# Optimization experiments

Hardware: AMD Instinct MI355X
Metric: run time of the kernel (lower is better)

## Reference

```python
import jax, jax.numpy as jnp
import numpy as np

E = 16      # num_experts
K = 2       # top-k
C = 1280    # capacity = ceil(8192*2/16*1.25)


def setup_inputs() -> dict:
    key = jax.random.key(0)
    ks = jax.random.split(key, 7)
    B, T, D, F, DFF = 4, 2048, 1024, 512, 512
    s = 0.02
    return {
        "hidden_state": jax.random.normal(ks[0], (B, T, D), jnp.float32),
        "router_w": jax.random.normal(ks[1], (D, E), jnp.float32) * s,
        "shared_gate_w": jax.random.normal(ks[2], (D, 1), jnp.float32) * s,
        "w1": jax.random.normal(ks[3], (E, D, F), jnp.float32) * s,
        "w2": jax.random.normal(ks[4], (E, F, D), jnp.float32) * s,
        "sw1": jax.random.normal(ks[5], (D, DFF), jnp.float32) * s,
        "sw2": jax.random.normal(ks[6], (DFF, D), jnp.float32) * s,
    }


def reference(hidden_state, router_w, shared_gate_w, w1, w2, sw1, sw2):
    B, T, D = hidden_state.shape
    N = B * T
    # Router: softmax over expert logits + shared sigmoid gate
    logits = jnp.einsum("btd,de->bte", hidden_state, router_w)
    scores = jax.nn.softmax(logits, axis=-1)                      # [B,T,E]
    g_shared = jax.nn.sigmoid(jnp.einsum("btd,do->bto", hidden_state, shared_gate_w))

    topk_vals, topk_idx = jax.lax.top_k(scores, K)                # [B,T,K]
    x = hidden_state.reshape(N, D)
    token_for_route = jnp.repeat(jnp.arange(N), K)                # [N*K]
    expert_for_route = topk_idx.reshape(-1)                       # [N*K]
    gate_for_route = topk_vals.reshape(-1)                        # [N*K]

    # Stable sort by expert (jnp.argsort is stable)
    order = jnp.argsort(expert_for_route)
    expert_sorted = expert_for_route[order]
    token_sorted = token_for_route[order]
    gate_sorted = gate_for_route[order]
    x_sorted = x[token_sorted]                                    # [N*K, D]

    counts = jnp.bincount(expert_sorted, length=E)
    starts = jnp.cumsum(counts) - counts
    r = jnp.arange(N * K)
    positions = r - starts[expert_sorted]                         # slot within expert
    keep = (positions < C) & (gate_sorted != 0)
    p_idx = jnp.clip(positions, 0, C - 1)

    # Scatter kept tokens into fixed-capacity buffers; dropped routes go to dummy row E
    e_safe = jnp.where(keep, expert_sorted, E)
    p_safe = jnp.where(keep, p_idx, 0)
    buf = jnp.zeros((E + 1, C, D), x.dtype).at[e_safe, p_safe].set(
        jnp.where(keep[:, None], x_sorted, 0.0)
    )
    expert_inputs = buf[:E]                                       # [E,C,D]

    # Batched expert FFN (exact GELU, matching torch default)
    h = jax.nn.gelu(jnp.einsum("ech,ehf->ecf", expert_inputs, w1), approximate=False)
    expert_outputs = jnp.einsum("ecf,efh->ech", h, w2)            # [E,C,D]

    gate_eff = jnp.where(keep, gate_sorted, 0.0)
    y_sorted = expert_outputs[expert_sorted, p_idx] * gate_eff[:, None]

    # Combine: scatter-add back to tokens
    y_out = jnp.zeros((N, D), x.dtype).at[token_sorted].add(y_sorted).reshape(B, T, D)

    # Shared expert path
    shared_out = (jax.nn.gelu(x @ sw1, approximate=False) @ sw2).reshape(B, T, D)
    y_out = y_out + g_shared * shared_out

    # Stats (no attention_mask path)
    load_counts = jnp.bincount(expert_for_route, length=E)
    load = load_counts / (load_counts.sum() + 1e-12)
    importance = scores.mean(axis=(0, 1))
    return (y_out, importance, load)
```

## Files before the change

### kernel.cpp

```cpp
#include <hip/hip_runtime.h>
#include <hip/hip_bf16.h>
#include <math.h>

#define N_TOK 8192
#define DIM 1024
#define NEXP 16
#define CAP 1280
#define FDIM 512
#define NROUTE (N_TOK * 2)
#define NCHUNK 64
#define ECAP (NEXP * CAP)
#define TOTROW (ECAP + N_TOK)

typedef __hip_bfloat16 bf16;
typedef unsigned short ushort_t;
typedef __attribute__((ext_vector_type(8))) short bf16x8;
typedef __attribute__((ext_vector_type(4))) float f32x4;

__device__ __forceinline__ float gelu_fast(float x) {
    float u = 1.5957691216057308f * (x + 0.044715f * x * x * x);
    return x / (1.f + __expf(-u));
}

__device__ __forceinline__ float bf2f(unsigned short u) {
    union { float f; unsigned int i; } v; v.i = ((unsigned int)u) << 16; return v.f;
}

__device__ __forceinline__ unsigned short f2b(float f) {
    union { __hip_bfloat16 h; unsigned short u; } v;
    v.h = __float2bfloat16(f);
    return v.u;
}

__device__ __forceinline__ void gload16(const void* g, void* l) {
    __builtin_amdgcn_global_load_lds(
        (const __attribute__((address_space(1))) unsigned int*)g,
        (__attribute__((address_space(3))) unsigned int*)l,
        16, 0, 0);
}

__device__ __forceinline__ int swz_addr16(int r, int q) {
    return ((r >> 1) << 3) + ((r & 1) << 2) + (q ^ ((r >> 1) & 3));
}

#define PREP_RTR_BLOCKS 2048
#define PREP_NWG (PREP_RTR_BLOCKS + 2176)
__global__ __launch_bounds__(256) void prep_kernel(
    const float* __restrict__ x, const float* __restrict__ rw,
    const float* __restrict__ sgw,
    const float* __restrict__ w1, const float* __restrict__ w2,
    const float* __restrict__ sw1, const float* __restrict__ sw2,
    float* __restrict__ scores,
    int* __restrict__ topk_idx,
    float* __restrict__ topk_val,
    float* __restrict__ g_shared,
    ushort_t* __restrict__ x_bf,
    ushort_t* __restrict__ w1t, ushort_t* __restrict__ w2t,
    ushort_t* __restrict__ sw1t, ushort_t* __restrict__ sw2t)
{
    __shared__ union {
        ushort_t tileB[64][129];
        struct {
            float xl[4][1028];
            float racc[4][4][4][4];
            float g[4][4];
        } r;
    } sm;

    if (blockIdx.x < PREP_RTR_BLOCKS) {
        int tid = threadIdx.x;
        int w = tid >> 6;
        int lane = tid & 63;
        int tok0 = blockIdx.x * 4;

        {
            int dq = w * 256 + lane * 4;
            float4 gv = *reinterpret_cast<const float4*>(sgw + dq);
#pragma unroll
            for (int tt = 0; tt < 4; ++tt) {
                const float* xr = x + (size_t)(tok0 + tt) * DIM + dq;
                float4 xv = *reinterpret_cast<const float4*>(xr);
                *reinterpret_cast<float4*>(&sm.r.xl[tt][dq]) = xv;
                ushort4 o;
                o.x = f2b(xv.x); o.y = f2b(xv.y); o.z = f2b(xv.z); o.w = f2b(xv.w);
                *reinterpret_cast<ushort4*>(x_bf + (size_t)(tok0 + tt) * DIM + dq) = o;
                float dg = xv.x * gv.x + xv.y * gv.y + xv.z * gv.z + xv.w * gv.w;
#pragma unroll
                for (int m = 1; m < 64; m <<= 1) dg += __shfl_xor(dg, m, 64);
                if (lane == 0) sm.r.g[w][tt] = dg;
            }
        }
        __syncthreads();

        int tok = lane >> 4;
        int dup = (lane >> 2) & 3;
        int e4 = lane & 3;
        {
            int base_d = w * 256 + dup * 64;
            const float* rwb = rw + (size_t)base_d * NEXP + e4 * 4;
            float4 a0 = {0,0,0,0}, a1 = {0,0,0,0}, a2 = {0,0,0,0}, a3 = {0,0,0,0};
#pragma unroll 4
            for (int i = 0; i < 16; ++i) {
                float4 xv = *reinterpret_cast<const float4*>(&sm.r.xl[tok][base_d + i * 4]);
                const float* rp = rwb + (size_t)i * 4 * NEXP;
                float4 w0 = *reinterpret_cast<const float4*>(rp);
                float4 w1v = *reinterpret_cast<const float4*>(rp + NEXP);
                float4 w2v = *reinterpret_cast<const float4*>(rp + 2 * NEXP);
                float4 w3v = *reinterpret_cast<const float4*>(rp + 3 * NEXP);
                a0.x += xv.x * w0.x;  a0.y += xv.x * w0.y;  a0.z += xv.x * w0.z;  a0.w += xv.x * w0.w;
                a1.x += xv.y * w1v.x; a1.y += xv.y * w1v.y; a1.z += xv.y * w1v.z; a1.w += xv.y * w1v.w;
                a2.x += xv.z * w2v.x; a2.y += xv.z * w2v.y; a2.z += xv.z * w2v.z; a2.w += xv.z * w2v.w;
                a3.x += xv.w * w3v.x; a3.y += xv.w * w3v.y; a3.z += xv.w * w3v.z; a3.w += xv.w * w3v.w;
            }
            float s0 = (a0.x + a1.x) + (a2.x + a3.x);
            float s1 = (a0.y + a1.y) + (a2.y + a3.y);
            float s2 = (a0.z + a1.z) + (a2.z + a3.z);
            float s3 = (a0.w + a1.w) + (a2.w + a3.w);
            s0 += __shfl_xor(s0, 4, 64);  s0 += __shfl_xor(s0, 8, 64);
            s1 += __shfl_xor(s1, 4, 64);  s1 += __shfl_xor(s1, 8, 64);
            s2 += __shfl_xor(s2, 4, 64);  s2 += __shfl_xor(s2, 8, 64);
            s3 += __shfl_xor(s3, 4, 64);  s3 += __shfl_xor(s3, 8, 64);
            if (dup == 0) {
                sm.r.racc[w][tok][e4][0] = s0;
                sm.r.racc[w][tok][e4][1] = s1;
                sm.r.racc[w][tok][e4][2] = s2;
                sm.r.racc[w][tok][e4][3] = s3;
            }
        }
        __syncthreads();

        if (tid >= 16) return;
        int tk = tid >> 2;
        int eq = tid & 3;
        int token = tok0 + tk;
        float L0 = sm.r.racc[0][tk][eq][0] + sm.r.racc[1][tk][eq][0]
                 + sm.r.racc[2][tk][eq][0] + sm.r.racc[3][tk][eq][0];
        float L1 = sm.r.racc[0][tk][eq][1] + sm.r.racc[1][tk][eq][1]
                 + sm.r.racc[2][tk][eq][1] + sm.r.racc[3][tk][eq][1];
        float L2 = sm.r.racc[0][tk][eq][2] + sm.r.racc[1][tk][eq][2]
                 + sm.r.racc[2][tk][eq][2] + sm.r.racc[3][tk][eq][2];
        float L3 = sm.r.racc[0][tk][eq][3] + sm.r.racc[1][tk][eq][3]
                 + sm.r.racc[2][tk][eq][3] + sm.r.racc[3][tk][eq][3];

        float mx = fmaxf(fmaxf(L0, L1), fmaxf(L2, L3));
        mx = fmaxf(mx, __shfl_xor(mx, 1, 4));
        mx = fmaxf(mx, __shfl_xor(mx, 2, 4));
        float P0 = expf(L0 - mx), P1 = expf(L1 - mx);
        float P2 = expf(L2 - mx), P3 = expf(L3 - mx);
        float s = (P0 + P1) + (P2 + P3);
        s += __shfl_xor(s, 1, 4);
        s += __shfl_xor(s, 2, 4);
        float inv = 1.f / s;
        P0 *= inv; P1 *= inv; P2 *= inv; P3 *= inv;

        float4 Pv = {P0, P1, P2, P3};
        *reinterpret_cast<float4*>(scores + (size_t)token * NEXP + eq * 4) = Pv;

        int base = eq * 4;
        float v = P0; int idx = base;
        if (P1 > v) { v = P1; idx = base + 1; }
        if (P2 > v) { v = P2; idx = base + 2; }
        if (P3 > v) { v = P3; idx = base + 3; }
#pragma unroll
        for (int m = 1; m < 4; m <<= 1) {
            float vo = __shfl_xor(v, m, 4);
            int io = __shfl_xor(idx, m, 4);
            if (vo > v || (vo == v && io < idx)) { v = vo; idx = io; }
        }
        int i0 = idx; float v0 = v;
        float q0 = (base + 0 == i0) ? -1.f : P0;
        float q1 = (base + 1 == i0) ? -1.f : P1;
        float q2 = (base + 2 == i0) ? -1.f : P2;
        float q3 = (base + 3 == i0) ? -1.f : P3;
        v = q0; idx = base;
        if (q1 > v) { v = q1; idx = base + 1; }
        if (q2 > v) { v = q2; idx = base + 2; }
        if (q3 > v) { v = q3; idx = base + 3; }
#pragma unroll
        for (int m = 1; m < 4; m <<= 1) {
            float vo = __shfl_xor(v, m, 4);
            int io = __shfl_xor(idx, m, 4);
            if (vo > v || (vo == v && io < idx)) { v = vo; idx = io; }
        }
        if (eq == 0) {
            topk_idx[2 * token] = i0; topk_idx[2 * token + 1] = idx;
            topk_val[2 * token] = v0; topk_val[2 * token + 1] = v;
            float ag = (sm.r.g[0][tk] + sm.r.g[1][tk]) + (sm.r.g[2][tk] + sm.r.g[3][tk]);
            g_shared[token] = 1.f / (1.f + expf(-ag));
        }
        return;
    }

    int bx = blockIdx.x - PREP_RTR_BLOCKS;
    const float* src; ushort_t* dst; int K, N, kt, nt;
    if (bx < 1024) {
        int e = bx >> 6, r = bx & 63;
        K = 1024; N = 512; kt = r >> 3; nt = r & 7;
        src = w1 + (size_t)e * K * N; dst = w1t + (size_t)e * K * N;
    } else if (bx < 2048) {
        int b2 = bx - 1024, e = b2 >> 6, r = b2 & 63;
        K = 512; N = 1024; kt = r >> 4; nt = r & 15;
        src = w2 + (size_t)e * K * N; dst = w2t + (size_t)e * K * N;
    } else if (bx < 2112) {
        int r = bx - 2048;
        K = 1024; N = 512; kt = r >> 3; nt = r & 7;
        src = sw1; dst = sw1t;
    } else {
        int r = bx - 2112;
        K = 512; N = 1024; kt = r >> 4; nt = r & 15;
        src = sw2; dst = sw2t;
    }
    int t = threadIdx.x;
#pragma unroll 4
    for (int i = 0; i < 8; ++i) {
        int u = t + 256 * i;
        int r = u >> 4;
        int c4 = (u & 15) * 4;
        float4 v = *reinterpret_cast<const float4*>(
            src + (size_t)(kt * 128 + r) * N + nt * 64 + c4);
        sm.tileB[c4 + 0][r] = f2b(v.x);
        sm.tileB[c4 + 1][r] = f2b(v.y);
        sm.tileB[c4 + 2][r] = f2b(v.z);
        sm.tileB[c4 + 3][r] = f2b(v.w);
    }
    __syncthreads();
#pragma unroll 4
    for (int i2 = 0; i2 < 4; ++i2) {
        int u = t + 256 * i2;
        int n = u >> 4;
        int kc = (u & 15) * 8;
        bf16x8 o;
#pragma unroll
        for (int j = 0; j < 8; ++j) o[j] = (short)sm.tileB[n][kc + j];
        *reinterpret_cast<bf16x8*>(dst + (size_t)(nt * 64 + n) * K + kt * 128 + kc) = o;
    }
}

__global__ __launch_bounds__(256) void hist_kernel(
    const int* __restrict__ topk_idx, int* __restrict__ chunk_hist)
{
    __shared__ int h[NEXP];
    int tid = threadIdx.x;
    if (tid < NEXP) h[tid] = 0;
    __syncthreads();
    int r = blockIdx.x * 256 + tid;
    atomicAdd(&h[topk_idx[r]], 1);
    __syncthreads();
    if (tid < NEXP) chunk_hist[blockIdx.x * NEXP + tid] = h[tid];
}

__global__ __launch_bounds__(64) void scan_kernel(
    const int* __restrict__ chunk_hist, int* __restrict__ chunk_off,
    int* __restrict__ counts_cap, float* __restrict__ out_tail)
{
    int e = threadIdx.x;
    if (e >= NEXP) return;
    int run = 0;
    for (int b = 0; b < NCHUNK; ++b) {
        chunk_off[b * NEXP + e] = run;
        run += chunk_hist[b * NEXP + e];
    }
    counts_cap[e] = run < CAP ? run : CAP;
    out_tail[NEXP + e] = (float)((double)run / 16384.0);
}

__global__ __launch_bounds__(256) void assign_kernel(
    const int* __restrict__ topk_idx, const float* __restrict__ topk_val,
    const int* __restrict__ chunk_off,
    int* __restrict__ route_slot, int* __restrict__ slot_token)
{
    __shared__ int wave_cnt[4][NEXP];
    int tid = threadIdx.x;
    int lane = tid & 63;
    int w = tid >> 6;
    int r = blockIdx.x * 256 + tid;
    int e = topk_idx[r];
    float gate = topk_val[r];
    int rank_w = 0;
#pragma unroll
    for (int e16 = 0; e16 < NEXP; ++e16) {
        unsigned long long bal = __ballot(e == e16);
        if (e == e16) rank_w = __popcll(bal & ((1ull << lane) - 1ull));
        if (lane == 0) wave_cnt[w][e16] = __popcll(bal);
    }
    __syncthreads();
    int rank = rank_w;
#pragma unroll
    for (int w2 = 0; w2 < 3; ++w2)
        if (w2 < w) rank += wave_cnt[w2][e];
    int pos = chunk_off[blockIdx.x * NEXP + e] + rank;
    int slot = -1;
    if (pos < CAP && gate != 0.f) {
        slot = e * CAP + pos;
        slot_token[slot] = r >> 1;
    }
    route_slot[r] = slot;
}

__global__ __launch_bounds__(256) void importance_kernel(
    const float* __restrict__ scores, float* __restrict__ out_tail)
{
    __shared__ float red[256];
    int e = blockIdx.x;
    float s = 0.f;
    for (int t = threadIdx.x; t < N_TOK; t += 256) s += scores[t * NEXP + e];
    red[threadIdx.x] = s;
    __syncthreads();
    for (int st = 128; st > 0; st >>= 1) {
        if (threadIdx.x < st) red[threadIdx.x] += red[threadIdx.x + st];
        __syncthreads();
    }
    if (threadIdx.x == 0) out_tail[e] = red[0] / (float)N_TOK;
}

#define G1_GX (NEXP * 5 + N_TOK / 256)
#define G1_NWG (G1_GX * (FDIM / 128))
__global__ __launch_bounds__(512) void gemm1_mfma(
    const ushort_t* __restrict__ x_bf,
    const ushort_t* __restrict__ w1t,
    const ushort_t* __restrict__ sw1t,
    const int* __restrict__ slot_token,
    const int* __restrict__ counts_cap,
    ushort_t* __restrict__ h_buf)
{
    __shared__ ushort_t As[3][256 * 32];
    __shared__ ushort_t Bs[3][128 * 32];

    int flat = blockIdx.x;
    int wg = (flat & 7) * (G1_NWG / 8) + (flat >> 3);
    int by = wg & 3;
    int bxg = wg >> 2;

    int g, rb;
    if (bxg < NEXP * 5) { g = bxg / 5; rb = bxg % 5; }
    else { g = NEXP; rb = bxg - NEXP * 5; }
    int Mg = (g < NEXP) ? counts_cap[g] : N_TOK;
    int m0 = rb * 256;
    if (m0 >= Mg) return;
    const ushort_t* Bt = (g < NEXP) ? (w1t + (size_t)g * DIM * FDIM) : sw1t;
    int n0 = by * 128;
    int t = threadIdx.x;

    const ushort_t* asrc[2];
    const ushort_t* bsrc;
#pragma unroll
    for (int i = 0; i < 2; ++i) {
        int s = t + i * 512;
        int lr = ((s >> 3) << 1) | ((s >> 2) & 1);
        int qq = (s & 3) ^ ((s >> 3) & 3);
        int row = m0 + lr;
        const ushort_t* base;
        if (g < NEXP) {
            int tok = (row < Mg) ? slot_token[g * CAP + row] : 0;
            if ((unsigned)tok >= N_TOK) tok = 0;
            base = x_bf + (size_t)tok * DIM;
        } else {
            base = x_bf + (size_t)row * DIM;
        }
        asrc[i] = base + qq * 8;
    }
    {
        int s = t;
        int lr = ((s >> 3) << 1) | ((s >> 2) & 1);
        int qq = (s & 3) ^ ((s >> 3) & 3);
        bsrc = Bt + (size_t)(n0 + lr) * DIM + qq * 8;
    }

    int lane = t & 63;
    int w = t >> 6;
    int wm = (w & 3) * 64, wn = (w >> 2) * 64;
    int l15 = lane & 15, q = lane >> 4;

    int aoff[4], boff[4];
#pragma unroll
    for (int m = 0; m < 4; ++m) aoff[m] = swz_addr16(wm + m * 16 + l15, q) << 3;
#pragma unroll
    for (int n = 0; n < 4; ++n) boff[n] = swz_addr16(wn + n * 16 + l15, q) << 3;

    f32x4 acc[4][4];
#pragma unroll
    for (int m = 0; m < 4; ++m)
#pragma unroll
        for (int n = 0; n < 4; ++n) acc[m][n] = (f32x4){0.f, 0.f, 0.f, 0.f};

    auto STAGE = [&](int buf, int koff) {
        gload16(asrc[0] + koff, &As[buf][t * 8]);
        gload16(asrc[1] + koff, &As[buf][t * 8 + 4096]);
        gload16(bsrc + koff, &Bs[buf][t * 8]);
    };

    const int NSTEP = DIM / 32;
    STAGE(0, 0);
    STAGE(1, 32);
    asm volatile("s_waitcnt vmcnt(3)" ::: "memory");
    __builtin_amdgcn_s_barrier();
    asm volatile("" ::: "memory");

    int cur = 0, b2 = 2;
    for (int kt = 0; kt < NSTEP; ++kt) {
        if (kt + 2 < NSTEP) STAGE(b2, (kt + 2) * 32);
        const ushort_t* asb = &As[cur][0];
        const ushort_t* bsb = &Bs[cur][0];
        bf16x8 af[4], bfr[4];
#pragma unroll
        for (int m = 0; m < 4; ++m)
            af[m] = *reinterpret_cast<const bf16x8*>(asb + aoff[m]);
#pragma unroll
        for (int n = 0; n < 4; ++n)
            bfr[n] = *reinterpret_cast<const bf16x8*>(bsb + boff[n]);
        __builtin_amdgcn_s_setprio(1);
#pragma unroll
        for (int m = 0; m < 4; ++m)
#pragma unroll
            for (int n = 0; n < 4; ++n)
                acc[m][n] = __builtin_amdgcn_mfma_f32_16x16x32_bf16(
                    af[m], bfr[n], acc[m][n], 0, 0, 0);
        __builtin_amdgcn_s_setprio(0);
        if (kt + 1 < NSTEP) {
            if (kt + 2 < NSTEP) asm volatile("s_waitcnt vmcnt(3)" ::: "memory");
            else                asm volatile("s_waitcnt vmcnt(0)" ::: "memory");
            __builtin_amdgcn_s_barrier();
            asm volatile("" ::: "memory");
        }
        cur = (cur == 2) ? 0 : cur + 1;
        b2  = (b2 == 2) ? 0 : b2 + 1;
    }

    size_t obase = ((g < NEXP) ? (size_t)g * CAP : (size_t)ECAP) + m0;
#pragma unroll
    for (int m = 0; m < 4; ++m) {
#pragma unroll
        for (int r = 0; r < 4; ++r) {
            int grow = wm + m * 16 + q * 4 + r;
            ushort_t* orow = h_buf + (obase + grow) * FDIM + n0 + wn + l15;
#pragma unroll
            for (int n = 0; n < 4; ++n)
                orow[n * 16] = f2b(gelu_fast(acc[m][n][r]));
        }
    }
}

#define G2_NWG (G1_GX * (DIM / 128))
__global__ __launch_bounds__(512) void gemm2_mfma(
    const ushort_t* __restrict__ h_buf,
    const ushort_t* __restrict__ w2t,
    const ushort_t* __restrict__ sw2t,
    const int* __restrict__ counts_cap,
    const float* __restrict__ g_shared,
    ushort_t* __restrict__ out_buf,
    ushort_t* __restrict__ sh_out)
{
    __shared__ ushort_t As[2][256 * 32];
    __shared__ ushort_t Bs[2][128 * 32];

    int flat = blockIdx.x;
    int wg = (flat & 7) * (G2_NWG / 8) + (flat >> 3);
    int by = wg & 7;
    int bxg = wg >> 3;

    int g, rb;
    if (bxg < NEXP * 5) { g = bxg / 5; rb = bxg % 5; }
    else { g = NEXP; rb = bxg - NEXP * 5; }
    int Mg = (g < NEXP) ? counts_cap[g] : N_TOK;
    int m0 = rb * 256;
    if (m0 >= Mg) return;
    size_t abase = ((g < NEXP) ? (size_t)g * CAP : (size_t)ECAP) + m0;
    const ushort_t* Bt = (g < NEXP) ? (w2t + (size_t)g * FDIM * DIM) : sw2t;
    int n0 = by * 128;
    int t = threadIdx.x;

    const ushort_t* asrc[2];
    const ushort_t* bsrc;
#pragma unroll
    for (int i = 0; i < 2; ++i) {
        int s = t + i * 512;
        int lr = ((s >> 3) << 1) | ((s >> 2) & 1);
        int qq = (s & 3) ^ ((s >> 3) & 3);
        asrc[i] = h_buf + (abase + lr) * FDIM + qq * 8;
    }
    {
        int s = t;
        int lr = ((s >> 3) << 1) | ((s >> 2) & 1);
        int qq = (s & 3) ^ ((s >> 3) & 3);
        bsrc = Bt + (size_t)(n0 + lr) * FDIM + qq * 8;
    }

    int lane = t & 63;
    int w = t >> 6;
    int wm = (w & 3) * 64, wn = (w >> 2) * 64;
    int l15 = lane & 15, q = lane >> 4;

    int aoff[4], boff[4];
#pragma unroll
    for (int m = 0; m < 4; ++m) aoff[m] = swz_addr16(wm + m * 16 + l15, q) << 3;
#pragma unroll
    for (int n = 0; n < 4; ++n) boff[n] = swz_addr16(wn + n * 16 + l15, q) << 3;

    f32x4 acc[4][4];
#pragma unroll
    for (int m = 0; m < 4; ++m)
#pragma unroll
        for (int n = 0; n < 4; ++n) acc[m][n] = (f32x4){0.f, 0.f, 0.f, 0.f};

    auto STAGE = [&](int buf, int koff) {
        gload16(asrc[0] + koff, &As[buf][t * 8]);
        gload16(asrc[1] + koff, &As[buf][t * 8 + 4096]);
        gload16(bsrc + koff, &Bs[buf][t * 8]);
    };

    const int NSTEP = FDIM / 32;
    STAGE(0, 0);
    __syncthreads();

    int cur = 0;
    for (int kt = 0; kt < NSTEP; ++kt) {
        if (kt + 1 < NSTEP) STAGE(cur ^ 1, (kt + 1) * 32);
        const ushort_t* asb = &As[cur][0];
        const ushort_t* bsb = &Bs[cur][0];
        bf16x8 af[4], bfr[4];
#pragma unroll
        for (int m = 0; m < 4; ++m)
            af[m] = *reinterpret_cast<const bf16x8*>(asb + aoff[m]);
#pragma unroll
        for (int n = 0; n < 4; ++n)
            bfr[n] = *reinterpret_cast<const bf16x8*>(bsb + boff[n]);
        __builtin_amdgcn_s_setprio(1);
#pragma unroll
        for (int m = 0; m < 4; ++m)
#pragma unroll
            for (int n = 0; n < 4; ++n)
                acc[m][n] = __builtin_amdgcn_mfma_f32_16x16x32_bf16(
                    af[m], bfr[n], acc[m][n], 0, 0, 0);
        __builtin_amdgcn_s_setprio(0);
        __syncthreads();
        cur ^= 1;
    }

    if (g < NEXP) {
#pragma unroll
        for (int m = 0; m < 4; ++m) {
#pragma unroll
            for (int r = 0; r < 4; ++r) {
                int grow = wm + m * 16 + q * 4 + r;
                ushort_t* orow = out_buf + (abase + grow) * DIM + n0 + wn + l15;
#pragma unroll
                for (int n = 0; n < 4; ++n)
                    orow[n * 16] = f2b(acc[m][n][r]);
            }
        }
    } else {
#pragma unroll
        for (int m = 0; m < 4; ++m) {
#pragma unroll
            for (int r = 0; r < 4; ++r) {
                int tok = m0 + wm + m * 16 + q * 4 + r;
                float gs = g_shared[tok];
                ushort_t* orow = sh_out + (size_t)tok * DIM + n0 + wn + l15;
#pragma unroll
                for (int n = 0; n < 4; ++n)
                    orow[n * 16] = f2b(gs * acc[m][n][r]);
            }
        }
    }
}

__global__ __launch_bounds__(256) void combine_kernel(
    const ushort_t* __restrict__ out_buf, const ushort_t* __restrict__ sh_out,
    const int* __restrict__ route_slot, const float* __restrict__ topk_val,
    float* __restrict__ y)
{
    int token = blockIdx.x;
    int c = threadIdx.x * 4;
    ushort4 sv = *reinterpret_cast<const ushort4*>(sh_out + (size_t)token * DIM + c);
    float y0 = bf2f(sv.x), y1 = bf2f(sv.y), y2 = bf2f(sv.z), y3 = bf2f(sv.w);
#pragma unroll
    for (int k = 0; k < 2; ++k) {
        int s = route_slot[2 * token + k];
        if (s >= 0) {
            float gate = topk_val[2 * token + k];
            ushort4 rv = *reinterpret_cast<const ushort4*>(out_buf + (size_t)s * DIM + c);
            y0 += gate * bf2f(rv.x); y1 += gate * bf2f(rv.y);
            y2 += gate * bf2f(rv.z); y3 += gate * bf2f(rv.w);
        }
    }
    float4 o; o.x = y0; o.y = y1; o.z = y2; o.w = y3;
    *reinterpret_cast<float4*>(y + (size_t)token * DIM + c) = o;
}

extern "C" void kernel_launch(void* const* d_in, const int* in_sizes, int n_in,
                              void* d_out, int out_size, void* d_ws, size_t ws_size,
                              hipStream_t stream) {
    const float* x   = (const float*)d_in[0];
    const float* rw  = (const float*)d_in[1];
    const float* sgw = (const float*)d_in[2];
    const float* w1  = (const float*)d_in[3];
    const float* w2  = (const float*)d_in[4];
    const float* sw1 = (const float*)d_in[5];
    const float* sw2 = (const float*)d_in[6];
    float* y = (float*)d_out;
    float* out_tail = y + (size_t)N_TOK * DIM;

    size_t off = 0;
    char* wsb = (char*)d_ws;
    auto alloc = [&](size_t bytes) -> void* {
        void* p = wsb + off;
        off += (bytes + 255) & ~(size_t)255;
        return p;
    };
    float*    scores     = (float*)alloc((size_t)N_TOK * NEXP * 4);
    int*      topk_idx   = (int*)alloc((size_t)NROUTE * 4);
    float*    topk_val   = (float*)alloc((size_t)NROUTE * 4);
    float*    g_shared   = (float*)alloc((size_t)N_TOK * 4);
    int*      chunk_hist = (int*)alloc((size_t)NCHUNK * NEXP * 4);
    int*      chunk_off  = (int*)alloc((size_t)NCHUNK * NEXP * 4);
    int*      counts_cap = (int*)alloc((size_t)NEXP * 4);
    int*      route_slot = (int*)alloc((size_t)NROUTE * 4);
    int*      slot_token = (int*)alloc((size_t)ECAP * 4);
    ushort_t* out_buf    = (ushort_t*)alloc((size_t)ECAP * DIM * 2);
    ushort_t* x_bf       = (ushort_t*)alloc((size_t)N_TOK * DIM * 2);
    ushort_t* sh_out     = x_bf;
    ushort_t* w1t        = (ushort_t*)alloc((size_t)NEXP * DIM * FDIM * 2);
    ushort_t* w2t        = (ushort_t*)alloc((size_t)NEXP * DIM * FDIM * 2);
    ushort_t* sw1t       = (ushort_t*)alloc((size_t)DIM * FDIM * 2);
    ushort_t* sw2t       = (ushort_t*)alloc((size_t)DIM * FDIM * 2);
    ushort_t* h_buf      = (ushort_t*)alloc((size_t)TOTROW * FDIM * 2);
    (void)ws_size; (void)in_sizes; (void)n_in; (void)out_size;

    prep_kernel<<<PREP_NWG, 256, 0, stream>>>(
        x, rw, sgw, w1, w2, sw1, sw2,
        scores, topk_idx, topk_val, g_shared, x_bf, w1t, w2t, sw1t, sw2t);
    hist_kernel<<<NCHUNK, 256, 0, stream>>>(topk_idx, chunk_hist);
    scan_kernel<<<1, 64, 0, stream>>>(chunk_hist, chunk_off, counts_cap, out_tail);
    assign_kernel<<<NCHUNK, 256, 0, stream>>>(topk_idx, topk_val, chunk_off, route_slot, slot_token);
    importance_kernel<<<NEXP, 256, 0, stream>>>(scores, out_tail);

    gemm1_mfma<<<G1_NWG, 512, 0, stream>>>(x_bf, w1t, sw1t, slot_token, counts_cap, h_buf);
    gemm2_mfma<<<G2_NWG, 512, 0, stream>>>(h_buf, w2t, sw2t, counts_cap, g_shared, out_buf, sh_out);

    combine_kernel<<<N_TOK, 256, 0, stream>>>(out_buf, sh_out, route_slot, topk_val, y);
}
```

Baseline: 150.9 us.

## Move w2/sw2 bf16 transpose into gemm1 launch and pad router LDS layout

The w2 and sw2 fp32-to-bf16 transposes move out of the prep kernel and into extra workgroups appended to the gemm1 launch, so that conversion work overlaps with the GEMM and prep gets shorter. The extra blocks share LDS with the GEMM tiles through a union. Separately, the router's per-token x staging in LDS is padded to 68 floats per 64-element chunk to reduce bank conflicts on the float4 reads. The appended blocks run last in grid order, so they may land in the tail of gemm1 instead of overlapping with it.

```diff
diff --git a/kernel.cpp b/kernel.cpp
--- a/kernel.cpp
+++ b/kernel.cpp
@@ -17,6 +17,9 @@
 typedef __attribute__((ext_vector_type(8))) short bf16x8;
 typedef __attribute__((ext_vector_type(4))) float f32x4;
 
+#define XL_CH 68
+#define XL_TOK 1104
+
 __device__ __forceinline__ float gelu_fast(float x) {
     float u = 1.5957691216057308f * (x + 0.044715f * x * x * x);
     return x / (1.f + __expf(-u));
@@ -44,24 +47,22 @@
 }
 
 #define PREP_RTR_BLOCKS 2048
-#define PREP_NWG (PREP_RTR_BLOCKS + 2176)
+#define PREP_NWG (PREP_RTR_BLOCKS + 1088)
 __global__ __launch_bounds__(256) void prep_kernel(
     const float* __restrict__ x, const float* __restrict__ rw,
     const float* __restrict__ sgw,
-    const float* __restrict__ w1, const float* __restrict__ w2,
-    const float* __restrict__ sw1, const float* __restrict__ sw2,
+    const float* __restrict__ w1, const float* __restrict__ sw1,
     float* __restrict__ scores,
     int* __restrict__ topk_idx,
     float* __restrict__ topk_val,
     float* __restrict__ g_shared,
     ushort_t* __restrict__ x_bf,
-    ushort_t* __restrict__ w1t, ushort_t* __restrict__ w2t,
-    ushort_t* __restrict__ sw1t, ushort_t* __restrict__ sw2t)
+    ushort_t* __restrict__ w1t, ushort_t* __restrict__ sw1t)
 {
     __shared__ union {
         ushort_t tileB[64][129];
         struct {
-            float xl[4][1028];
+            float xl[4 * XL_TOK];
             float racc[4][4][4][4];
             float g[4][4];
         } r;
@@ -75,12 +76,13 @@
 
         {
             int dq = w * 256 + lane * 4;
+            int xoff = (dq >> 6) * XL_CH + (dq & 63);
             float4 gv = *reinterpret_cast<const float4*>(sgw + dq);
 #pragma unroll
             for (int tt = 0; tt < 4; ++tt) {
                 const float* xr = x + (size_t)(tok0 + tt) * DIM + dq;
                 float4 xv = *reinterpret_cast<const float4*>(xr);
-                *reinterpret_cast<float4*>(&sm.r.xl[tt][dq]) = xv;
+                *reinterpret_cast<float4*>(&sm.r.xl[tt * XL_TOK + xoff]) = xv;
                 ushort4 o;
                 o.x = f2b(xv.x); o.y = f2b(xv.y); o.z = f2b(xv.z); o.w = f2b(xv.w);
                 *reinterpret_cast<ushort4*>(x_bf + (size_t)(tok0 + tt) * DIM + dq) = o;
@@ -97,11 +99,12 @@
         int e4 = lane & 3;
         {
             int base_d = w * 256 + dup * 64;
+            const float* xc = &sm.r.xl[tok * XL_TOK + (base_d >> 6) * XL_CH];
             const float* rwb = rw + (size_t)base_d * NEXP + e4 * 4;
             float4 a0 = {0,0,0,0}, a1 = {0,0,0,0}, a2 = {0,0,0,0}, a3 = {0,0,0,0};
 #pragma unroll 4
             for (int i = 0; i < 16; ++i) {
-                float4 xv = *reinterpret_cast<const float4*>(&sm.r.xl[tok][base_d + i * 4]);
+                float4 xv = *reinterpret_cast<const float4*>(xc + i * 4);
                 const float* rp = rwb + (size_t)i * 4 * NEXP;
                 float4 w0 = *reinterpret_cast<const float4*>(rp);
                 float4 w1v = *reinterpret_cast<const float4*>(rp + NEXP);
@@ -197,18 +200,10 @@
         int e = bx >> 6, r = bx & 63;
         K = 1024; N = 512; kt = r >> 3; nt = r & 7;
         src = w1 + (size_t)e * K * N; dst = w1t + (size_t)e * K * N;
-    } else if (bx < 2048) {
-        int b2 = bx - 1024, e = b2 >> 6, r = b2 & 63;
-        K = 512; N = 1024; kt = r >> 4; nt = r & 15;
-        src = w2 + (size_t)e * K * N; dst = w2t + (size_t)e * K * N;
-    } else if (bx < 2112) {
-        int r = bx - 2048;
+    } else {
+        int r = bx - 1024;
         K = 1024; N = 512; kt = r >> 3; nt = r & 7;
         src = sw1; dst = sw1t;
-    } else {
-        int r = bx - 2112;
-        K = 512; N = 1024; kt = r >> 4; nt = r & 15;
-        src = sw2; dst = sw2t;
     }
     int t = threadIdx.x;
 #pragma unroll 4
@@ -315,16 +310,64 @@
 
 #define G1_GX (NEXP * 5 + N_TOK / 256)
 #define G1_NWG (G1_GX * (FDIM / 128))
-__global__ __launch_bounds__(512) void gemm1_mfma(
+#define G1X_NWG (G1_NWG + 1088)
+__global__ __launch_bounds__(512) void gemm1x_kernel(
     const ushort_t* __restrict__ x_bf,
     const ushort_t* __restrict__ w1t,
     const ushort_t* __restrict__ sw1t,
     const int* __restrict__ slot_token,
     const int* __restrict__ counts_cap,
-    ushort_t* __restrict__ h_buf)
-{
-    __shared__ ushort_t As[3][256 * 32];
-    __shared__ ushort_t Bs[3][128 * 32];
+    ushort_t* __restrict__ h_buf,
+    const float* __restrict__ w2, const float* __restrict__ sw2,
+    ushort_t* __restrict__ w2t, ushort_t* __restrict__ sw2t)
+{
+    __shared__ union {
+        struct {
+            ushort_t As[3][256 * 32];
+            ushort_t Bs[3][128 * 32];
+        } g;
+        ushort_t tileB[64][129];
+    } sm;
+
+    int t = threadIdx.x;
+
+    if (blockIdx.x >= G1_NWG) {
+        int bx = blockIdx.x - G1_NWG;
+        const float* src; ushort_t* dst; int K, N, kt, nt;
+        if (bx < 1024) {
+            int e = bx >> 6, r = bx & 63;
+            K = 512; N = 1024; kt = r >> 4; nt = r & 15;
+            src = w2 + (size_t)e * K * N; dst = w2t + (size_t)e * K * N;
+        } else {
+            int r = bx - 1024;
+            K = 512; N = 1024; kt = r >> 4; nt = r & 15;
+            src = sw2; dst = sw2t;
+        }
+#pragma unroll 4
+        for (int i = 0; i < 4; ++i) {
+            int u = t + 512 * i;
+            int r = u >> 4;
+            int c4 = (u & 15) * 4;
+            float4 v = *reinterpret_cast<const float4*>(
+                src + (size_t)(kt * 128 + r) * N + nt * 64 + c4);
+            sm.tileB[c4 + 0][r] = f2b(v.x);
+            sm.tileB[c4 + 1][r] = f2b(v.y);
+            sm.tileB[c4 + 2][r] = f2b(v.z);
+            sm.tileB[c4 + 3][r] = f2b(v.w);
+        }
+        __syncthreads();
+#pragma unroll 2
+        for (int i2 = 0; i2 < 2; ++i2) {
+            int u = t + 512 * i2;
+            int n = u >> 4;
+            int kc = (u & 15) * 8;
+            bf16x8 o;
+#pragma unroll
+            for (int j = 0; j < 8; ++j) o[j] = (short)sm.tileB[n][kc + j];
+            *reinterpret_cast<bf16x8*>(dst + (size_t)(nt * 64 + n) * K + kt * 128 + kc) = o;
+        }
+        return;
+    }
 
     int flat = blockIdx.x;
     int wg = (flat & 7) * (G1_NWG / 8) + (flat >> 3);
@@ -339,7 +382,6 @@
     if (m0 >= Mg) return;
     const ushort_t* Bt = (g < NEXP) ? (w1t + (size_t)g * DIM * FDIM) : sw1t;
     int n0 = by * 128;
-    int t = threadIdx.x;
 
     const ushort_t* asrc[2];
     const ushort_t* bsrc;
@@ -384,9 +426,9 @@
         for (int n = 0; n < 4; ++n) acc[m][n] = (f32x4){0.f, 0.f, 0.f, 0.f};
 
     auto STAGE = [&](int buf, int koff) {
-        gload16(asrc[0] + koff, &As[buf][t * 8]);
-        gload16(asrc[1] + koff, &As[buf][t * 8 + 4096]);
-        gload16(bsrc + koff, &Bs[buf][t * 8]);
+        gload16(asrc[0] + koff, &sm.g.As[buf][t * 8]);
+        gload16(asrc[1] + koff, &sm.g.As[buf][t * 8 + 4096]);
+        gload16(bsrc + koff, &sm.g.Bs[buf][t * 8]);
     };
 
     const int NSTEP = DIM / 32;
@@ -399,8 +441,8 @@
     int cur = 0, b2 = 2;
     for (int kt = 0; kt < NSTEP; ++kt) {
         if (kt + 2 < NSTEP) STAGE(b2, (kt + 2) * 32);
-        const ushort_t* asb = &As[cur][0];
-        const ushort_t* bsb = &Bs[cur][0];
+        const ushort_t* asb = &sm.g.As[cur][0];
+        const ushort_t* bsb = &sm.g.Bs[cur][0];
         bf16x8 af[4], bfr[4];
 #pragma unroll
         for (int m = 0; m < 4; ++m)
@@ -627,14 +669,15 @@
     (void)ws_size; (void)in_sizes; (void)n_in; (void)out_size;
 
     prep_kernel<<<PREP_NWG, 256, 0, stream>>>(
-        x, rw, sgw, w1, w2, sw1, sw2,
-        scores, topk_idx, topk_val, g_shared, x_bf, w1t, w2t, sw1t, sw2t);
+        x, rw, sgw, w1, sw1,
+        scores, topk_idx, topk_val, g_shared, x_bf, w1t, sw1t);
     hist_kernel<<<NCHUNK, 256, 0, stream>>>(topk_idx, chunk_hist);
     scan_kernel<<<1, 64, 0, stream>>>(chunk_hist, chunk_off, counts_cap, out_tail);
     assign_kernel<<<NCHUNK, 256, 0, stream>>>(topk_idx, topk_val, chunk_off, route_slot, slot_token);
     importance_kernel<<<NEXP, 256, 0, stream>>>(scores, out_tail);
 
-    gemm1_mfma<<<G1_NWG, 512, 0, stream>>>(x_bf, w1t, sw1t, slot_token, counts_cap, h_buf);
+    gemm1x_kernel<<<G1X_NWG, 512, 0, stream>>>(
+        x_bf, w1t, sw1t, slot_token, counts_cap, h_buf, w2, sw2, w2t, sw2t);
     gemm2_mfma<<<G2_NWG, 512, 0, stream>>>(h_buf, w2t, sw2t, counts_cap, g_shared, out_buf, sh_out);
 
     combine_kernel<<<N_TOK, 256, 0, stream>>>(out_buf, sh_out, route_slot, topk_val, y);
```

Result: faster. 146.7 us (-2.8%).
